# Kernel tuning notes

Measured on AMD Instinct MI355X. Metric: run time of the kernel, lower is better.

## Reference

```python
import jax, jax.numpy as jnp
import numpy as np

N_HEADS = 16
LOCAL_WINDOW = 512
ROPE_BASE = 10000.0


def _rotate_half(x):
    # interleaved rotate: out[..., 2i] = -x[..., 2i+1], out[..., 2i+1] = x[..., 2i]
    x1 = x[..., 0::2]
    x2 = x[..., 1::2]
    return jnp.stack((-x2, x1), axis=-1).reshape(x.shape)


def _rope_cache(T, hd, dtype):
    half = hd // 2
    inv_freq = 1.0 / (ROPE_BASE ** (jnp.arange(half, dtype=dtype) / half))
    t = jnp.arange(T, dtype=dtype)
    freqs = t[:, None] * inv_freq[None, :]  # [T, half]
    cos = jnp.repeat(jnp.cos(freqs), 2, axis=-1)  # [T, hd]
    sin = jnp.repeat(jnp.sin(freqs), 2, axis=-1)
    return cos, sin


def setup_inputs() -> dict:
    key = jax.random.key(0)
    k1, k2, k3, k4 = jax.random.split(key, 4)
    B, T, C = 2, 2048, 1024
    x = jax.random.normal(k1, (B, T, C), dtype=jnp.float32)
    Wqkv = jax.random.normal(k2, (3 * C, C), dtype=jnp.float32) * 0.02
    Wproj = jax.random.normal(k3, (C, C), dtype=jnp.float32) * 0.02
    bproj = jax.random.normal(k4, (C,), dtype=jnp.float32) * 0.02
    return {"x": x, "Wqkv": Wqkv, "Wproj": Wproj, "bproj": bproj}


def reference(x, Wqkv, Wproj, bproj):
    B, T, C = x.shape
    H = N_HEADS
    hd = C // H
    qkv = (x @ Wqkv.T).reshape(B, T, 3, H, hd).transpose(2, 0, 3, 1, 4)  # [3,B,H,T,hd]
    q, k, v = qkv[0], qkv[1], qkv[2]
    cos, sin = _rope_cache(T, hd, x.dtype)
    cos = cos[None, None]  # [1,1,T,hd]
    sin = sin[None, None]
    q = q * cos + _rotate_half(q) * sin
    k = k * cos + _rotate_half(k) * sin
    scale = 1.0 / jnp.sqrt(jnp.asarray(hd, dtype=x.dtype))
    scores = jnp.einsum('bhqd,bhkd->bhqk', q, k) * scale  # [B,H,T,T]
    i = jnp.arange(T)[:, None]
    j = jnp.arange(T)[None, :]
    allow = (j <= i) & (jnp.abs(i - j) <= LOCAL_WINDOW)  # causal & local band
    scores = jnp.where(allow[None, None], scores, jnp.asarray(-jnp.inf, dtype=x.dtype))
    attn = jax.nn.softmax(scores, axis=-1)
    y = jnp.einsum('bhqk,bhkd->bhqd', attn, v)  # [B,H,T,hd]
    y = y.transpose(0, 2, 1, 3).reshape(B, T, C)
    return y @ Wproj.T + bproj
```

## Files before the change

### kernel.cpp

```cpp
#include <hip/hip_runtime.h>
#include <math.h>

#define B_   2
#define T_   2048
#define C_   1024
#define H_   16
#define HD_  64
#define WIN_ 512
#define BT_  (B_ * T_)

typedef __bf16 bf16x8 __attribute__((ext_vector_type(8)));
typedef float  f32x4  __attribute__((ext_vector_type(4)));
typedef unsigned int u32x2 __attribute__((ext_vector_type(2)));
typedef unsigned short u16x8 __attribute__((ext_vector_type(8)));

__device__ __forceinline__ f32x4 mfma16(bf16x8 a, bf16x8 b, f32x4 c) {
    return __builtin_amdgcn_mfma_f32_16x16x32_bf16(a, b, c, 0, 0, 0);
}
__device__ __forceinline__ unsigned short f2b(float f) {
    __bf16 h = (__bf16)f;
    unsigned short u;
    __builtin_memcpy(&u, &h, 2);
    return u;
}
__device__ __forceinline__ void async_copy16(__bf16* lds, const __bf16* g) {
    __builtin_amdgcn_global_load_lds(
        (const __attribute__((address_space(1))) void*)g,
        (__attribute__((address_space(3))) void*)lds,
        16, 0, 0);
}

#define TR16(dst, va, OFFLIT) \
    asm volatile("ds_read_b64_tr_b16 %0, %1 offset:" OFFLIT : "=v"(dst) : "v"(va))

__device__ __forceinline__ bf16x8 combine_tr(u32x2 a, u32x2 b) {
    union { unsigned u[4]; bf16x8 v; } x;
    x.u[0] = a[0]; x.u[1] = a[1]; x.u[2] = b[0]; x.u[3] = b[1];
    return x.v;
}

__global__ void prep_k(const float* __restrict__ x, const float* __restrict__ Wqkv,
                       const float* __restrict__ Wproj,
                       __bf16* __restrict__ xb, __bf16* __restrict__ Wqkvb,
                       __bf16* __restrict__ Wprojb,
                       float* __restrict__ cosT, float* __restrict__ sinT) {
    const int gid = blockIdx.x * 256 + threadIdx.x;
    const int N0 = BT_ * 1024 / 8;
    const int N1 = N0 + 3072 * 1024 / 8;
    const int N2 = N1 + 1024 * 1024 / 8;
    const int N3 = N2 + T_ * 32 / 8;
    if (gid < N2) {
        const float* src; __bf16* dst; int off;
        if (gid < N0)      { src = x;     dst = xb;     off = gid; }
        else if (gid < N1) { src = Wqkv;  dst = Wqkvb;  off = gid - N0; }
        else               { src = Wproj; dst = Wprojb; off = gid - N1; }
        float4 a = *(const float4*)&src[(size_t)off * 8];
        float4 b = *(const float4*)&src[(size_t)off * 8 + 4];
        bf16x8 o;
        o[0] = (__bf16)a.x; o[1] = (__bf16)a.y; o[2] = (__bf16)a.z; o[3] = (__bf16)a.w;
        o[4] = (__bf16)b.x; o[5] = (__bf16)b.y; o[6] = (__bf16)b.z; o[7] = (__bf16)b.w;
        *(bf16x8*)&dst[(size_t)off * 8] = o;
    } else if (gid < N3) {
        const int r = gid - N2;
        #pragma unroll
        for (int e = 0; e < 8; ++e) {
            int idx = r * 8 + e;
            int t = idx >> 5, j = idx & 31;
            float inv = powf(10000.0f, -(float)j / 32.0f);
            float f = (float)t * inv;
            cosT[idx] = cosf(f);
            sinT[idx] = sinf(f);
        }
    }
}

template<bool OUT_BF16, bool ROPE>
__global__ __launch_bounds__(256) void gemm_bt_mfma(
        const __bf16* __restrict__ A, const __bf16* __restrict__ Bm,
        const float* __restrict__ bias, void* __restrict__ Cv,
        int M, int N, int K,
        const float* __restrict__ cosT, const float* __restrict__ sinT)
{
    __shared__ __bf16 As[2][128 * 32];
    __shared__ __bf16 Bs[2][128 * 32];
    const int tid  = threadIdx.x;
    const int w    = tid >> 6;
    const int lane = tid & 63;
    const int c    = lane & 15;
    const int g    = lane >> 4;
    const int bm0  = blockIdx.y * 128;
    const int bn0  = blockIdx.x * 128;
    const int wm0  = (w >> 1) * 64;
    const int wn0  = (w & 1) * 64;

    f32x4 acc[4][4] = {};

    auto stage = [&](int buf, int k0) {
        #pragma unroll
        for (int it = 0; it < 2; ++it) {
            int slot = it * 256 + tid;
            int r    = slot >> 2;
            int c8   = (slot & 3) * 8;
            async_copy16(&As[buf][slot * 8], &A[(size_t)(bm0 + r) * K + k0 + c8]);
            async_copy16(&Bs[buf][slot * 8], &Bm[(size_t)(bn0 + r) * K + k0 + c8]);
        }
    };

    stage(0, 0);
    int cur = 0;
    for (int k0 = 0; k0 < K; k0 += 32) {
        __syncthreads();
        if (k0 + 32 < K) stage(cur ^ 1, k0 + 32);
        bf16x8 af[4], bfr[4];
        #pragma unroll
        for (int m = 0; m < 4; ++m)
            af[m] = *(const bf16x8*)&As[cur][(wm0 + m * 16 + c) * 32 + g * 8];
        #pragma unroll
        for (int n = 0; n < 4; ++n)
            bfr[n] = *(const bf16x8*)&Bs[cur][(wn0 + n * 16 + c) * 32 + g * 8];
        #pragma unroll
        for (int m = 0; m < 4; ++m)
            #pragma unroll
            for (int n = 0; n < 4; ++n)
                acc[m][n] = mfma16(af[m], bfr[n], acc[m][n]);
        cur ^= 1;
    }

    if (ROPE) {
        #pragma unroll
        for (int m = 0; m < 4; ++m) {
            #pragma unroll
            for (int r2 = 0; r2 < 4; ++r2) {
                const int row = bm0 + wm0 + m * 16 + g * 4 + r2;
                const int t = row & (T_ - 1);
                #pragma unroll
                for (int n = 0; n < 4; ++n) {
                    const int cbase = bn0 + wn0 + n * 16;
                    const int cc = cbase + c;
                    float v = acc[m][n][r2];
                    float outv;
                    if (cbase < 2048) {
                        float prt = __shfl_xor(v, 1);
                        int jj = (cc & 63) >> 1;
                        float cs = cosT[t * 32 + jj];
                        float sn = sinT[t * 32 + jj];
                        outv = (cc & 1) ? (v * cs + prt * sn) : (v * cs - prt * sn);
                    } else {
                        outv = v;
                    }
                    ((__bf16*)Cv)[(size_t)row * N + cc] = (__bf16)outv;
                }
            }
        }
    } else {
        #pragma unroll
        for (int m = 0; m < 4; ++m) {
            int rr = bm0 + wm0 + m * 16 + g * 4;
            #pragma unroll
            for (int n = 0; n < 4; ++n) {
                int cc = bn0 + wn0 + n * 16 + c;
                float bv = (!OUT_BF16 && bias) ? bias[cc] : 0.f;
                #pragma unroll
                for (int r2 = 0; r2 < 4; ++r2) {
                    float v = acc[m][n][r2] + bv;
                    if (OUT_BF16) ((__bf16*)Cv)[(size_t)(rr + r2) * N + cc] = (__bf16)v;
                    else          ((float*)Cv)[(size_t)(rr + r2) * N + cc] = v;
                }
            }
        }
    }
}

__global__ __launch_bounds__(256) void attn_k(const __bf16* __restrict__ qkv,
                                              __bf16* __restrict__ y)
{
    __shared__ __align__(16) unsigned short Ks[64 * 72];
    __shared__ __align__(16) unsigned short Ps[64 * 72];
    __shared__ __align__(16) unsigned short Vs[4 * 1040];

    const int tid  = threadIdx.x;
    const int lane = tid & 63;
    const int w    = tid >> 6;
    const int c    = lane & 15;
    const int g    = lane >> 4;

    const int bid = blockIdx.x;
    const int swz = (bid & 7) * 128 + (bid >> 3);
    const int q0 = (swz & 31) * 64;
    const int hb = swz >> 5;
    const int h  = hb & 15;
    const int b  = hb >> 4;

    bf16x8 qa[2];
    {
        const int qrow = q0 + w * 16 + c;
        const __bf16* qp = qkv + (size_t)(b * T_ + qrow) * 3072 + h * 64 + g * 8;
        bf16x8 r0 = *(const bf16x8*)qp;
        bf16x8 r1 = *(const bf16x8*)(qp + 32);
        #pragma unroll
        for (int e = 0; e < 8; ++e) {
            qa[0][e] = (__bf16)((float)r0[e] * 0.125f);
            qa[1][e] = (__bf16)((float)r1[e] * 0.125f);
        }
    }

    float m_run[4] = {-1e30f, -1e30f, -1e30f, -1e30f};
    float l_run[4] = {0.f, 0.f, 0.f, 0.f};
    f32x4 o[4] = {};

    unsigned vs_lane;
    {
        auto* p3 = (__attribute__((address_space(3))) const unsigned short*)Vs;
        vs_lane = (unsigned)(unsigned long long)p3 + (unsigned)(g * 256 + c * 8);
    }

    const int r0s = tid >> 3,          d80 = (tid & 7) * 8;
    const int r1s = (tid + 256) >> 3,  d81 = d80;
    const size_t kbase = (size_t)(b * T_) * 3072 + 1024 + h * 64;

    const int j_start = (q0 >= WIN_) ? (q0 - WIN_) : 0;

    u16x8 kr0, kr1, vr0, vr1;
    {
        const __bf16* p0 = qkv + kbase + (size_t)(j_start + r0s) * 3072 + d80;
        const __bf16* p1 = qkv + kbase + (size_t)(j_start + r1s) * 3072 + d81;
        kr0 = *(const u16x8*)p0;  vr0 = *(const u16x8*)(p0 + 1024);
        kr1 = *(const u16x8*)p1;  vr1 = *(const u16x8*)(p1 + 1024);
    }

    for (int j0 = j_start; j0 <= q0; j0 += 64) {
        __syncthreads();
        {
            union { u16x8 v; ushort4 h[2]; } u;
            u.v = kr0;
            *(ushort4*)&Ks[r0s * 72 + d80]     = u.h[0];
            *(ushort4*)&Ks[r0s * 72 + d80 + 4] = u.h[1];
            u.v = kr1;
            *(ushort4*)&Ks[r1s * 72 + d81]     = u.h[0];
            *(ushort4*)&Ks[r1s * 72 + d81 + 4] = u.h[1];
            *(u16x8*)&Vs[(d80 >> 4) * 1040 + r0s * 16 + (d80 & 15)] = vr0;
            *(u16x8*)&Vs[(d81 >> 4) * 1040 + r1s * 16 + (d81 & 15)] = vr1;
        }
        __syncthreads();

        if (j0 + 64 <= q0) {
            const __bf16* p0 = qkv + kbase + (size_t)(j0 + 64 + r0s) * 3072 + d80;
            const __bf16* p1 = qkv + kbase + (size_t)(j0 + 64 + r1s) * 3072 + d81;
            kr0 = *(const u16x8*)p0;  vr0 = *(const u16x8*)(p0 + 1024);
            kr1 = *(const u16x8*)p1;  vr1 = *(const u16x8*)(p1 + 1024);
        }

        f32x4 sc[4];
        __builtin_amdgcn_s_setprio(1);
        #pragma unroll
        for (int nt = 0; nt < 4; ++nt) {
            const bf16x8 b0 = *(const bf16x8*)&Ks[(nt * 16 + c) * 72 + g * 8];
            const bf16x8 b1 = *(const bf16x8*)&Ks[(nt * 16 + c) * 72 + 32 + g * 8];
            f32x4 s = {0.f, 0.f, 0.f, 0.f};
            s = mfma16(qa[0], b0, s);
            s = mfma16(qa[1], b1, s);
            sc[nt] = s;
        }
        __builtin_amdgcn_s_setprio(0);

        const int rlo = q0 + w * 16;
        const bool need_mask = (j0 + 63 > rlo) || (rlo + 15 - j0 > WIN_);
        if (need_mask) {
            #pragma unroll
            for (int reg = 0; reg < 4; ++reg) {
                const int i_abs = rlo + g * 4 + reg;
                #pragma unroll
                for (int nt = 0; nt < 4; ++nt) {
                    int j_abs = j0 + nt * 16 + c;
                    bool ok = (j_abs <= i_abs) && (i_abs - j_abs <= WIN_);
                    sc[nt][reg] = ok ? sc[nt][reg] : -1e30f;
                }
            }
        }

        float pmax[4];
        #pragma unroll
        for (int reg = 0; reg < 4; ++reg) {
            float bm = fmaxf(fmaxf(sc[0][reg], sc[1][reg]), fmaxf(sc[2][reg], sc[3][reg]));
            #pragma unroll
            for (int off = 1; off < 16; off <<= 1)
                bm = fmaxf(bm, __shfl_xor(bm, off));
            pmax[reg] = bm;
        }
        int need = 0;
        #pragma unroll
        for (int reg = 0; reg < 4; ++reg)
            need |= (pmax[reg] > m_run[reg] + 8.f) ? 1 : 0;
        if (__any(need)) {
            #pragma unroll
            for (int reg = 0; reg < 4; ++reg) {
                float mn = fmaxf(m_run[reg], pmax[reg]);
                float corr = __expf(m_run[reg] - mn);
                m_run[reg] = mn;
                l_run[reg] *= corr;
                #pragma unroll
                for (int dt = 0; dt < 4; ++dt) o[dt][reg] *= corr;
            }
        }
        #pragma unroll
        for (int reg = 0; reg < 4; ++reg) {
            #pragma unroll
            for (int nt = 0; nt < 4; ++nt) {
                float p = __expf(sc[nt][reg] - m_run[reg]);
                l_run[reg] += p;
                Ps[(w * 16 + g * 4 + reg) * 72 + nt * 16 + c] = f2b(p);
            }
        }

        const bf16x8 pa0 = *(const bf16x8*)&Ps[(w * 16 + c) * 72 + g * 8];
        const bf16x8 pa1 = *(const bf16x8*)&Ps[(w * 16 + c) * 72 + 32 + g * 8];
        u32x2 t0[4], t1[4], t2[4], t3[4];
        #pragma unroll
        for (int dt = 0; dt < 4; ++dt) {
            unsigned va = vs_lane + dt * 2080;
            TR16(t0[dt], va, "0");
            TR16(t1[dt], va, "128");
            TR16(t2[dt], va, "1024");
            TR16(t3[dt], va, "1152");
        }
        asm volatile("s_waitcnt lgkmcnt(0)" ::: "memory");
        __builtin_amdgcn_sched_barrier(0);
        __builtin_amdgcn_s_setprio(1);
        #pragma unroll
        for (int dt = 0; dt < 4; ++dt) {
            bf16x8 vb0 = combine_tr(t0[dt], t1[dt]);
            bf16x8 vb1 = combine_tr(t2[dt], t3[dt]);
            o[dt] = mfma16(pa0, vb0, o[dt]);
            o[dt] = mfma16(pa1, vb1, o[dt]);
        }
        __builtin_amdgcn_s_setprio(0);
    }

    float inv_l[4];
    #pragma unroll
    for (int reg = 0; reg < 4; ++reg) {
        float L = l_run[reg];
        #pragma unroll
        for (int off = 1; off < 16; off <<= 1)
            L += __shfl_xor(L, off);
        inv_l[reg] = 1.f / L;
    }
    #pragma unroll
    for (int dt = 0; dt < 4; ++dt)
        #pragma unroll
        for (int reg = 0; reg < 4; ++reg) {
            size_t row = (size_t)(b * T_ + q0 + w * 16 + g * 4 + reg);
            y[row * 1024 + h * 64 + dt * 16 + c] = (__bf16)(o[dt][reg] * inv_l[reg]);
        }
}

extern "C" void kernel_launch(void* const* d_in, const int* in_sizes, int n_in,
                              void* d_out, int out_size, void* d_ws, size_t ws_size,
                              hipStream_t stream) {
    const float* x     = (const float*)d_in[0];
    const float* Wqkv  = (const float*)d_in[1];
    const float* Wproj = (const float*)d_in[2];
    const float* bproj = (const float*)d_in[3];
    float* out = (float*)d_out;

    char* p = (char*)d_ws;
    float*  cosT   = (float*)p;   p += (size_t)T_ * 32 * 4;
    float*  sinT   = (float*)p;   p += (size_t)T_ * 32 * 4;
    __bf16* xb     = (__bf16*)p;  p += (size_t)BT_ * 1024 * 2;
    __bf16* Wqkvb  = (__bf16*)p;  p += (size_t)3072 * 1024 * 2;
    __bf16* Wprojb = (__bf16*)p;  p += (size_t)1024 * 1024 * 2;
    __bf16* qkvb   = (__bf16*)p;  p += (size_t)BT_ * 3072 * 2;
    __bf16* yb     = (__bf16*)p;  p += (size_t)BT_ * 1024 * 2;

    const int nprep = (BT_ * 1024 + 3072 * 1024 + 1024 * 1024) / 8 + T_ * 32 / 8;
    prep_k<<<(nprep + 255) / 256, 256, 0, stream>>>(
        x, Wqkv, Wproj, xb, Wqkvb, Wprojb, cosT, sinT);

    dim3 g1(3072 / 128, BT_ / 128);
    gemm_bt_mfma<true, true><<<g1, 256, 0, stream>>>(
        xb, Wqkvb, nullptr, qkvb, BT_, 3072, 1024, cosT, sinT);

    attn_k<<<(T_ / 64) * H_ * B_, 256, 0, stream>>>(qkvb, yb);

    dim3 g2(1024 / 128, BT_ / 128);
    gemm_bt_mfma<false, false><<<g2, 256, 0, stream>>>(
        yb, Wprojb, bproj, out, BT_, 1024, 1024, nullptr, nullptr);
}
```

Measured before the change: 125.7 us.

## Replace QKV GEMM with 256x256-tile triple-buffered kernel with swizzled LDS

Adds a dedicated QKV projection GEMM using 256x256 tiles, 512 threads and a three-stage async global-to-LDS pipeline with explicit waitcnt and barrier scheduling. It also XOR-swizzles the LDS layout to avoid bank conflicts, remaps block indices for L2 locality, and raises MFMA priority with setprio. The aim is more data reuse per tile and better overlap of loads with MFMA for the larger GEMM. The trade-off is a large accumulator set (128 floats per lane) that raises register pressure, plus fewer blocks (192) on a device with many CUs. The output projection GEMM is simplified to a non-template fp32 path.

```diff
diff --git a/kernel.cpp b/kernel.cpp
--- a/kernel.cpp
+++ b/kernel.cpp
@@ -38,6 +38,8 @@
     x.u[0] = a[0]; x.u[1] = a[1]; x.u[2] = b[0]; x.u[3] = b[1];
     return x.v;
 }
+
+#define VMW(n) asm volatile("s_waitcnt vmcnt(" #n ")" ::: "memory")
 
 __global__ void prep_k(const float* __restrict__ x, const float* __restrict__ Wqkv,
                        const float* __restrict__ Wproj,
@@ -74,12 +76,129 @@
     }
 }
 
-template<bool OUT_BF16, bool ROPE>
+__global__ __launch_bounds__(512, 2) void gemm256_rope(
+        const __bf16* __restrict__ A, const __bf16* __restrict__ Bm,
+        __bf16* __restrict__ C, int M, int N, int K,
+        const float* __restrict__ cosT, const float* __restrict__ sinT)
+{
+    __shared__ __bf16 sA[3][256 * 32];
+    __shared__ __bf16 sB[3][256 * 32];
+
+    const int tid  = threadIdx.x;
+    const int w    = tid >> 6;
+    const int lane = tid & 63;
+    const int c    = lane & 15;
+    const int g    = lane >> 4;
+
+    const int nbx = N >> 8;
+    const int cpx = gridDim.x >> 3;
+    const int bid = blockIdx.x;
+    const int swz = (bid & 7) * cpx + (bid >> 3);
+    const int bm0 = (swz / nbx) << 8;
+    const int bn0 = (swz % nbx) << 8;
+
+    const int wm0 = (w >> 2) * 128;
+    const int wn0 = (w & 3) * 64;
+
+    auto stage = [&](const __bf16* base, __bf16* dstbuf, int brow0, int k0) {
+        #pragma unroll
+        for (int it = 0; it < 2; ++it) {
+            int s   = it * 512 + tid;
+            int row = s >> 2;
+            int col = ((s & 3) ^ ((row >> 1) & 3)) * 8;
+            async_copy16(&dstbuf[s * 8], &base[(size_t)(brow0 + row) * K + k0 + col]);
+        }
+    };
+    auto ldA = [&](const __bf16* buf, int m) -> bf16x8 {
+        int r = wm0 + m * 16 + c;
+        return *(const bf16x8*)&buf[r * 32 + ((g ^ ((r >> 1) & 3)) * 8)];
+    };
+    auto ldB = [&](const __bf16* buf, int n) -> bf16x8 {
+        int r = wn0 + n * 16 + c;
+        return *(const bf16x8*)&buf[r * 32 + ((g ^ ((r >> 1) & 3)) * 8)];
+    };
+
+    f32x4 acc[8][4] = {};
+    const int NT = K >> 5;
+
+    stage(A, sA[0], bm0, 0);  stage(Bm, sB[0], bn0, 0);
+    stage(A, sA[1], bm0, 32); stage(Bm, sB[1], bn0, 32);
+    VMW(4);
+    __builtin_amdgcn_sched_barrier(0);
+    __builtin_amdgcn_s_barrier();
+
+    int cons = 0;
+    for (int t = 0; t < NT; ++t) {
+        const int  sigma = t + 2;
+        const bool sv    = sigma < NT;
+        int fill = cons + 2; if (fill >= 3) fill -= 3;
+        const __bf16* cA = sA[cons];
+        const __bf16* cB = sB[cons];
+
+        bf16x8 bfr[4], af[4];
+        #pragma unroll
+        for (int n = 0; n < 4; ++n) bfr[n] = ldB(cB, n);
+        #pragma unroll
+        for (int i = 0; i < 4; ++i) af[i] = ldA(cA, i);
+        if (sv) stage(A, sA[fill], bm0, sigma * 32);
+        __builtin_amdgcn_s_barrier();
+        __builtin_amdgcn_s_setprio(1);
+        #pragma unroll
+        for (int i = 0; i < 4; ++i)
+            #pragma unroll
+            for (int n = 0; n < 4; ++n)
+                acc[i][n] = mfma16(af[i], bfr[n], acc[i][n]);
+        __builtin_amdgcn_s_setprio(0);
+        __builtin_amdgcn_s_barrier();
+
+        #pragma unroll
+        for (int i = 0; i < 4; ++i) af[i] = ldA(cA, 4 + i);
+        if (sv) stage(Bm, sB[fill], bn0, sigma * 32);
+        __builtin_amdgcn_s_barrier();
+        __builtin_amdgcn_s_setprio(1);
+        #pragma unroll
+        for (int i = 0; i < 4; ++i)
+            #pragma unroll
+            for (int n = 0; n < 4; ++n)
+                acc[4 + i][n] = mfma16(af[i], bfr[n], acc[4 + i][n]);
+        __builtin_amdgcn_s_setprio(0);
+        if (sv) { VMW(4); } else { VMW(0); }
+        __builtin_amdgcn_sched_barrier(0);
+        __builtin_amdgcn_s_barrier();
+        cons = (cons + 1 == 3) ? 0 : cons + 1;
+    }
+
+    #pragma unroll
+    for (int m = 0; m < 8; ++m) {
+        #pragma unroll
+        for (int r2 = 0; r2 < 4; ++r2) {
+            const int row = bm0 + wm0 + m * 16 + g * 4 + r2;
+            const int t = row & (T_ - 1);
+            #pragma unroll
+            for (int n = 0; n < 4; ++n) {
+                const int cbase = bn0 + wn0 + n * 16;
+                const int cc = cbase + c;
+                float v = acc[m][n][r2];
+                float outv;
+                if (cbase < 2048) {
+                    float prt = __shfl_xor(v, 1);
+                    int jj = (cc & 63) >> 1;
+                    float cs = cosT[t * 32 + jj];
+                    float sn = sinT[t * 32 + jj];
+                    outv = (cc & 1) ? (v * cs + prt * sn) : (v * cs - prt * sn);
+                } else {
+                    outv = v;
+                }
+                C[(size_t)row * N + cc] = (__bf16)outv;
+            }
+        }
+    }
+}
+
 __global__ __launch_bounds__(256) void gemm_bt_mfma(
         const __bf16* __restrict__ A, const __bf16* __restrict__ Bm,
-        const float* __restrict__ bias, void* __restrict__ Cv,
-        int M, int N, int K,
-        const float* __restrict__ cosT, const float* __restrict__ sinT)
+        const float* __restrict__ bias, float* __restrict__ Cv,
+        int M, int N, int K)
 {
     __shared__ __bf16 As[2][128 * 32];
     __shared__ __bf16 Bs[2][128 * 32];
@@ -126,47 +245,16 @@
         cur ^= 1;
     }
 
-    if (ROPE) {
-        #pragma unroll
-        for (int m = 0; m < 4; ++m) {
-            #pragma unroll
-            for (int r2 = 0; r2 < 4; ++r2) {
-                const int row = bm0 + wm0 + m * 16 + g * 4 + r2;
-                const int t = row & (T_ - 1);
-                #pragma unroll
-                for (int n = 0; n < 4; ++n) {
-                    const int cbase = bn0 + wn0 + n * 16;
-                    const int cc = cbase + c;
-                    float v = acc[m][n][r2];
-                    float outv;
-                    if (cbase < 2048) {
-                        float prt = __shfl_xor(v, 1);
-                        int jj = (cc & 63) >> 1;
-                        float cs = cosT[t * 32 + jj];
-                        float sn = sinT[t * 32 + jj];
-                        outv = (cc & 1) ? (v * cs + prt * sn) : (v * cs - prt * sn);
-                    } else {
-                        outv = v;
-                    }
-                    ((__bf16*)Cv)[(size_t)row * N + cc] = (__bf16)outv;
-                }
-            }
-        }
-    } else {
-        #pragma unroll
-        for (int m = 0; m < 4; ++m) {
-            int rr = bm0 + wm0 + m * 16 + g * 4;
-            #pragma unroll
-            for (int n = 0; n < 4; ++n) {
-                int cc = bn0 + wn0 + n * 16 + c;
-                float bv = (!OUT_BF16 && bias) ? bias[cc] : 0.f;
-                #pragma unroll
-                for (int r2 = 0; r2 < 4; ++r2) {
-                    float v = acc[m][n][r2] + bv;
-                    if (OUT_BF16) ((__bf16*)Cv)[(size_t)(rr + r2) * N + cc] = (__bf16)v;
-                    else          ((float*)Cv)[(size_t)(rr + r2) * N + cc] = v;
-                }
-            }
+    #pragma unroll
+    for (int m = 0; m < 4; ++m) {
+        int rr = bm0 + wm0 + m * 16 + g * 4;
+        #pragma unroll
+        for (int n = 0; n < 4; ++n) {
+            int cc = bn0 + wn0 + n * 16 + c;
+            float bv = bias ? bias[cc] : 0.f;
+            #pragma unroll
+            for (int r2 = 0; r2 < 4; ++r2)
+                Cv[(size_t)(rr + r2) * N + cc] = acc[m][n][r2] + bv;
         }
     }
 }
@@ -376,13 +464,11 @@
     prep_k<<<(nprep + 255) / 256, 256, 0, stream>>>(
         x, Wqkv, Wproj, xb, Wqkvb, Wprojb, cosT, sinT);
 
-    dim3 g1(3072 / 128, BT_ / 128);
-    gemm_bt_mfma<true, true><<<g1, 256, 0, stream>>>(
-        xb, Wqkvb, nullptr, qkvb, BT_, 3072, 1024, cosT, sinT);
+    gemm256_rope<<<(BT_ / 256) * (3072 / 256), 512, 0, stream>>>(
+        xb, Wqkvb, qkvb, BT_, 3072, 1024, cosT, sinT);
 
     attn_k<<<(T_ / 64) * H_ * B_, 256, 0, stream>>>(qkvb, yb);
 
     dim3 g2(1024 / 128, BT_ / 128);
-    gemm_bt_mfma<false, false><<<g2, 256, 0, stream>>>(
-        yb, Wprojb, bproj, out, BT_, 1024, 1024, nullptr, nullptr);
-}
+    gemm_bt_mfma<<<g2, 256, 0, stream>>>(yb, Wprojb, bproj, out, BT_, 1024, 1024);
+}
```

New measurement: 136.8 us. 8.8% more time.

## Triple-buffer GEMM LDS pipeline with XOR swizzle and explicit vmcnt waits

Applied to the files above, without the earlier changes.

Switches the bf16 MFMA GEMM main loop from double to triple buffering, prefetching two K-tiles ahead and using explicit s_waitcnt vmcnt plus a raw s_barrier instead of __syncthreads. It also XOR-swizzles the 16-byte column chunks in LDS to reduce bank conflicts on fragment reads, and raises wave priority around the MFMA block. The aim is to hide global-load latency and LDS conflicts, at the cost of 50% more LDS per block, which may lower occupancy. The hand-counted vmcnt values must match the number of outstanding async loads to stay correct.

```diff
diff --git a/kernel.cpp b/kernel.cpp
--- a/kernel.cpp
+++ b/kernel.cpp
@@ -38,6 +38,8 @@
     x.u[0] = a[0]; x.u[1] = a[1]; x.u[2] = b[0]; x.u[3] = b[1];
     return x.v;
 }
+
+#define VMW(n) asm volatile("s_waitcnt vmcnt(" #n ")" ::: "memory")
 
 __global__ void prep_k(const float* __restrict__ x, const float* __restrict__ Wqkv,
                        const float* __restrict__ Wproj,
@@ -81,8 +83,8 @@
         int M, int N, int K,
         const float* __restrict__ cosT, const float* __restrict__ sinT)
 {
-    __shared__ __bf16 As[2][128 * 32];
-    __shared__ __bf16 Bs[2][128 * 32];
+    __shared__ __bf16 sA[3][128 * 32];
+    __shared__ __bf16 sB[3][128 * 32];
     const int tid  = threadIdx.x;
     const int w    = tid >> 6;
     const int lane = tid & 63;
@@ -98,32 +100,47 @@
     auto stage = [&](int buf, int k0) {
         #pragma unroll
         for (int it = 0; it < 2; ++it) {
-            int slot = it * 256 + tid;
-            int r    = slot >> 2;
-            int c8   = (slot & 3) * 8;
-            async_copy16(&As[buf][slot * 8], &A[(size_t)(bm0 + r) * K + k0 + c8]);
-            async_copy16(&Bs[buf][slot * 8], &Bm[(size_t)(bn0 + r) * K + k0 + c8]);
+            int s   = it * 256 + tid;
+            int row = s >> 2;
+            int col = ((s & 3) ^ ((row >> 1) & 3)) * 8;
+            async_copy16(&sA[buf][s * 8], &A[(size_t)(bm0 + row) * K + k0 + col]);
+            async_copy16(&sB[buf][s * 8], &Bm[(size_t)(bn0 + row) * K + k0 + col]);
         }
     };
 
+    const int NT = K >> 5;
     stage(0, 0);
-    int cur = 0;
-    for (int k0 = 0; k0 < K; k0 += 32) {
-        __syncthreads();
-        if (k0 + 32 < K) stage(cur ^ 1, k0 + 32);
+    stage(1, 32);
+
+    for (int t = 0; t < NT; ++t) {
+        if (t + 1 < NT) { VMW(4); } else { VMW(0); }
+        __builtin_amdgcn_sched_barrier(0);
+        __builtin_amdgcn_s_barrier();
+        if (t + 2 < NT) {
+            int fill = t + 2; while (fill >= 3) fill -= 3;
+            stage(fill, (t + 2) * 32);
+        }
+        int cons = t; while (cons >= 3) cons -= 3;
+        const __bf16* cA = sA[cons];
+        const __bf16* cB = sB[cons];
         bf16x8 af[4], bfr[4];
         #pragma unroll
-        for (int m = 0; m < 4; ++m)
-            af[m] = *(const bf16x8*)&As[cur][(wm0 + m * 16 + c) * 32 + g * 8];
-        #pragma unroll
-        for (int n = 0; n < 4; ++n)
-            bfr[n] = *(const bf16x8*)&Bs[cur][(wn0 + n * 16 + c) * 32 + g * 8];
+        for (int m = 0; m < 4; ++m) {
+            int r = wm0 + m * 16 + c;
+            af[m] = *(const bf16x8*)&cA[r * 32 + ((g ^ ((r >> 1) & 3)) * 8)];
+        }
+        #pragma unroll
+        for (int n = 0; n < 4; ++n) {
+            int r = wn0 + n * 16 + c;
+            bfr[n] = *(const bf16x8*)&cB[r * 32 + ((g ^ ((r >> 1) & 3)) * 8)];
+        }
+        __builtin_amdgcn_s_setprio(1);
         #pragma unroll
         for (int m = 0; m < 4; ++m)
             #pragma unroll
             for (int n = 0; n < 4; ++n)
                 acc[m][n] = mfma16(af[m], bfr[n], acc[m][n]);
-        cur ^= 1;
+        __builtin_amdgcn_s_setprio(0);
     }
 
     if (ROPE) {
```

After: 125.6 us. About the same (-0.0%).
